# Kernel tuning notes

Measured on AMD Instinct MI355X. Metric: run time of the kernel, lower is better.

The kernel has to match this reference:

```python
import jax, jax.numpy as jnp
import numpy as np

D_MODEL = 96
D_STATE = 4
D_INNER = 192          # ssm_ratio * d_model
DT_RANK = 6            # ceil(d_model / 16)
K = 2                  # scan directions (fwd, reversed) over concatenated rgb||e sequence
D_CONV = 3
B, H, W = 2, 64, 64


def _layernorm(x, g, b, eps=1e-5):
    mu = jnp.mean(x, axis=-1, keepdims=True)
    var = jnp.mean((x - mu) ** 2, axis=-1, keepdims=True)
    return (x - mu) * jax.lax.rsqrt(var + eps) * g + b


def _dwconv(x, w, b):
    # x: [B, C, H, W], w: [C, 1, k, k] depthwise
    y = jax.lax.conv_general_dilated(
        x, w, window_strides=(1, 1), padding='SAME',
        feature_group_count=x.shape[1],
        dimension_numbers=('NCHW', 'OIHW', 'NCHW'))
    return y + b[None, :, None, None]


def setup_inputs() -> dict:
    key = jax.random.key(0)
    ks = jax.random.split(key, 16)
    f = lambda i, shape, s=0.02: jax.random.normal(ks[i], shape, dtype=jnp.float32) * s
    # dt_projs_bias mimics inverse-softplus of dt in [1e-3, 0.1]
    dt = jnp.exp(jax.random.uniform(ks[14], (K, D_INNER)) * (np.log(0.1) - np.log(0.001)) + np.log(0.001))
    inv_dt = dt + jnp.log(-jnp.expm1(-dt))
    return {
        'x_rgb': jax.random.normal(ks[0], (B, H, W, D_MODEL), jnp.float32),
        'x_e': jax.random.normal(ks[1], (B, H, W, D_MODEL), jnp.float32),
        'in_proj_w': f(2, (D_INNER, D_MODEL)),
        'in_proj_x_w': f(3, (D_INNER, D_MODEL)),
        'conv_w': f(4, (D_INNER, 1, D_CONV, D_CONV), 0.1),
        'conv_b': jnp.zeros((D_INNER,), jnp.float32),
        'conv_x_w': f(5, (D_INNER, 1, D_CONV, D_CONV), 0.1),
        'conv_x_b': jnp.zeros((D_INNER,), jnp.float32),
        'x_proj_weight': f(6, (K, DT_RANK + 2 * D_STATE, D_INNER)),
        'dt_projs_weight': f(7, (K, D_INNER, DT_RANK), DT_RANK ** -0.5),
        'dt_projs_bias': inv_dt.astype(jnp.float32),
        'A_logs': jnp.log(jnp.tile(jnp.arange(1, D_STATE + 1, dtype=jnp.float32)[None, :], (K * D_INNER, 1))),
        'Ds': jnp.ones((K * D_INNER,), jnp.float32),
        'ln1_g': jnp.ones((D_INNER,), jnp.float32), 'ln1_b': jnp.zeros((D_INNER,), jnp.float32),
        'ln2_g': jnp.ones((D_INNER,), jnp.float32), 'ln2_b': jnp.zeros((D_INNER,), jnp.float32),
        'out_proj_w': f(8, (D_MODEL, 2 * D_INNER)),
        'fc1_w1': f(9, (D_INNER // 16, D_INNER)), 'fc1_w2': f(10, (D_INNER, D_INNER // 16)),
        'fc2_w1': f(11, (D_INNER // 16, D_INNER)), 'fc2_w2': f(12, (D_INNER, D_INNER // 16)),
    }


def _mm_ss2d(x_rgb, x_e, in_proj_w, in_proj_x_w, conv_w, conv_b, conv_x_w, conv_x_b,
             x_proj_weight, dt_projs_weight, dt_projs_bias, A_logs, Ds,
             ln1_g, ln1_b, ln2_g, ln2_b, out_proj_w, fc1_w1, fc1_w2, fc2_w1, fc2_w2):
    # input projections (no bias)
    xr = x_rgb @ in_proj_w.T                       # [B,H,W,Di]
    xe = x_e @ in_proj_x_w.T
    xr_t = jnp.transpose(xr, (0, 3, 1, 2))         # [B,Di,H,W]
    xe_t = jnp.transpose(xe, (0, 3, 1, 2))
    xr_c = jax.nn.silu(_dwconv(xr_t, conv_w, conv_b))
    xe_c = jax.nn.silu(_dwconv(xe_t, conv_x_w, conv_x_b))

    Bb, Di, Hh, Ww = xr_c.shape
    HW = Hh * Ww
    # CrossScan_multimodal: concat rgb||e along sequence; K=2 = (forward, reversed)
    seq = jnp.concatenate([xr_c.reshape(Bb, Di, HW), xe_c.reshape(Bb, Di, HW)], axis=-1)  # [B,Di,2HW]
    xs = jnp.stack([seq, seq[..., ::-1]], axis=1)  # [B,K,Di,L]

    # projections for dt, B, C
    x_dbl = jnp.einsum('bkdl,kcd->bkcl', xs, x_proj_weight)
    dts, Bs, Cs = jnp.split(x_dbl, [DT_RANK, DT_RANK + D_STATE], axis=2)  # [B,K,R,L], [B,K,N,L] x2
    dts = jnp.einsum('bkrl,kdr->bkdl', dts, dt_projs_weight)
    delta = jax.nn.softplus(dts + dt_projs_bias.reshape(1, K, Di, 1))     # [B,K,Di,L]

    A = -jnp.exp(A_logs).reshape(K, Di, D_STATE)
    dA = jnp.exp(jnp.einsum('bkdl,kdn->bkdln', delta, A))                 # decay factors
    dBu = jnp.einsum('bkdl,bknl,bkdl->bkdln', delta, Bs, xs)              # driven input

    # S6 recurrence h_l = dA_l * h_{l-1} + dBu_l via parallel associative scan over L
    def combine(c1, c2):
        a1, b1 = c1
        a2, b2 = c2
        return a1 * a2, a2 * b1 + b2
    _, h = jax.lax.associative_scan(combine, (dA, dBu), axis=3)           # [B,K,Di,L,N]
    ys = jnp.einsum('bkdln,bknl->bkdl', h, Cs) + xs * Ds.reshape(1, K, Di, 1)

    # CrossMerge_multimodal: add reversed direction back, split modalities
    y = ys[:, 0] + ys[:, 1][..., ::-1]             # [B,Di,2HW]
    y_rgb = jnp.transpose(y[..., :HW], (0, 2, 1))  # [B,HW,Di]
    y_e = jnp.transpose(y[..., HW:], (0, 2, 1))
    y_rgb = _layernorm(y_rgb, ln1_g, ln1_b).reshape(Bb, Hh, Ww, Di)
    y_e = _layernorm(y_e, ln2_g, ln2_b).reshape(Bb, Hh, Ww, Di)

    # squeeze-excitation on pre-conv projected features
    sr = jnp.mean(xr_t, axis=(2, 3))               # [B,Di]
    se = jnp.mean(xe_t, axis=(2, 3))
    ex_r = jax.nn.sigmoid(jax.nn.silu(sr @ fc1_w1.T) @ fc1_w2.T)
    ex_e = jax.nn.sigmoid(jax.nn.silu(se @ fc2_w1.T) @ fc2_w2.T)
    y_rgb = y_rgb * ex_r[:, None, None, :]
    y_e = y_e * ex_e[:, None, None, :]

    yc = jnp.concatenate([y_rgb, y_e], axis=-1)    # [B,H,W,2Di]
    return yc @ out_proj_w.T                       # [B,H,W,d_model]


def reference(x_rgb, x_e, in_proj_w, in_proj_x_w, conv_w, conv_b, conv_x_w, conv_x_b,
              x_proj_weight, dt_projs_weight, dt_projs_bias, A_logs, Ds,
              ln1_g, ln1_b, ln2_g, ln2_b, out_proj_w, fc1_w1, fc1_w2, fc2_w1, fc2_w2):
    return _mm_ss2d(x_rgb, x_e, in_proj_w, in_proj_x_w, conv_w, conv_b, conv_x_w, conv_x_b,
                    x_proj_weight, dt_projs_weight, dt_projs_bias, A_logs, Ds,
                    ln1_g, ln1_b, ln2_g, ln2_b, out_proj_w, fc1_w1, fc1_w2, fc2_w1, fc2_w2)
```

## Files before the change

kernel.cpp:

```cpp
#include <hip/hip_runtime.h>
#include <math.h>

#define B_  2
#define H_  64
#define W_  64
#define HW  4096
#define DM  96
#define DI  192
#define NS  4
#define RK  6
#define KD  2
#define LL  8192

__device__ __forceinline__ float sigmoidf_(float x){ return 1.f/(1.f+__expf(-x)); }
__device__ __forceinline__ float4 rev4(float4 v){ return make_float4(v.w,v.z,v.y,v.x); }

__global__ void k_zero(float* __restrict__ p, int n){
  int i = blockIdx.x*256 + threadIdx.x;
  if (i < n) p[i] = 0.f;
}

__global__ __launch_bounds__(256) void k_inproj(
    const float* __restrict__ xrgb, const float* __restrict__ xe,
    const float* __restrict__ wr,   const float* __restrict__ we,
    float* __restrict__ xrt, float* __restrict__ xet, float* __restrict__ sr)
{
  __shared__ float lsW[DI*100];
  __shared__ float lsum[DI];
  const int mod = blockIdx.z, b = blockIdx.y;
  const int hw0 = blockIdx.x * 64;
  const float* x  = mod ? xe  : xrgb;
  const float* Wp = mod ? we  : wr;
  float* out      = mod ? xet : xrt;
  const int tid = threadIdx.x;
  for (int t = tid; t < DI*DM; t += 256){
    int di = t / DM, kk = t - di*DM;
    lsW[di*100 + kk] = Wp[t];
  }
  if (tid < DI) lsum[tid] = 0.f;
  const int cg = tid & 31, slot = tid >> 5;
  const int r0 = slot * 8;
  const float* xb = x + ((size_t)(b*HW) + hw0 + r0)*DM;
  float acc[8][6];
  #pragma unroll
  for (int i=0;i<8;i++)
    #pragma unroll
    for (int q=0;q<6;q++) acc[i][q]=0.f;
  __syncthreads();
  for (int kk4=0; kk4<DM/4; kk4++){
    float4 xv[8];
    #pragma unroll
    for (int i=0;i<8;i++) xv[i] = *(const float4*)(xb + (size_t)i*DM + kk4*4);
    #pragma unroll
    for (int q=0;q<6;q++){
      const float4 wv = *(const float4*)(&lsW[(cg+32*q)*100 + kk4*4]);
      #pragma unroll
      for (int i=0;i<8;i++){
        acc[i][q] = fmaf(xv[i].x, wv.x, acc[i][q]);
        acc[i][q] = fmaf(xv[i].y, wv.y, acc[i][q]);
        acc[i][q] = fmaf(xv[i].z, wv.z, acc[i][q]);
        acc[i][q] = fmaf(xv[i].w, wv.w, acc[i][q]);
      }
    }
  }
  #pragma unroll
  for (int q=0;q<6;q++){
    int di = cg + 32*q;
    float* ob = out + ((size_t)(b*DI + di))*HW + hw0 + r0;
    float ps = 0.f;
    #pragma unroll
    for (int i=0;i<8;i++){ ob[i] = acc[i][q]; ps += acc[i][q]; }
    atomicAdd(&lsum[di], ps);
  }
  __syncthreads();
  if (tid < DI) atomicAdd(&sr[((size_t)mod*B_ + b)*DI + tid], lsum[tid]);
}

__global__ __launch_bounds__(256) void k_conv(
    const float* __restrict__ xrt, const float* __restrict__ xet,
    const float* __restrict__ cwr, const float* __restrict__ cbr,
    const float* __restrict__ cwe, const float* __restrict__ cbe,
    float* __restrict__ seq)
{
  const int z = blockIdx.z; const int b = z >> 1, mod = z & 1;
  const int d = blockIdx.y;
  const float* in = (mod? xet:xrt) + ((size_t)b*DI + d)*HW;
  const float* wp = (mod? cwe:cwr) + d*9;
  const float  bias = (mod? cbe:cbr)[d];
  const int hw = blockIdx.x*256 + threadIdx.x;
  const int y = hw >> 6, x = hw & 63;
  float w[9];
  #pragma unroll
  for (int i=0;i<9;i++) w[i]=wp[i];
  float acc = bias;
  #pragma unroll
  for (int dy=-1;dy<=1;dy++){
    int yy = y+dy;
    if (yy<0||yy>=H_) continue;
    #pragma unroll
    for (int dx=-1;dx<=1;dx++){
      int xx = x+dx;
      if (xx<0||xx>=W_) continue;
      acc += in[yy*W_+xx]*w[(dy+1)*3 + dx+1];
    }
  }
  float v = acc * sigmoidf_(acc);
  seq[((size_t)b*DI + d)*LL + mod*HW + hw] = v;
}

__global__ void k_se(const float* __restrict__ sr,
                     const float* __restrict__ f11, const float* __restrict__ f12,
                     const float* __restrict__ f21, const float* __restrict__ f22,
                     float* __restrict__ ex)
{
  const int b = blockIdx.x, mod = blockIdx.y;
  const float* f1 = mod? f21:f11;
  const float* f2 = mod? f22:f12;
  __shared__ float s[DI];
  __shared__ float hid[12];
  const int t = threadIdx.x;
  s[t] = sr[((size_t)mod*B_ + b)*DI + t] * (1.f/HW);
  __syncthreads();
  if (t < 12){
    float a=0.f;
    for (int dd=0; dd<DI; dd++) a += f1[t*DI+dd]*s[dd];
    hid[t] = a * sigmoidf_(a);
  }
  __syncthreads();
  float a=0.f;
  #pragma unroll
  for (int h=0; h<12; h++) a += f2[t*12+h]*hid[h];
  ex[((size_t)mod*B_ + b)*DI + t] = sigmoidf_(a);
}

__global__ __launch_bounds__(256) void k_proj(
    const float* __restrict__ seq, const float* __restrict__ xpw,
    float* __restrict__ P)
{
  __shared__ float lw[14*DI];
  __shared__ float part[3][14][66];
  const int b = blockIdx.z, k = blockIdx.y;
  const int j0 = blockIdx.x*64;
  const int tid = threadIdx.x;
  const int jl = tid & 63, dq = tid >> 6;
  const int j = j0 + jl;
  for (int t = tid; t < 14*DI; t += 256) lw[t] = xpw[(size_t)k*14*DI + t];
  __syncthreads();
  float acc[14];
  #pragma unroll
  for (int c=0;c<14;c++) acc[c]=0.f;
  const float* sp = seq + (size_t)b*DI*LL + (size_t)(dq*48)*LL + j;
  const float* lwq = lw + dq*48;
  for (int dd=0; dd<48; dd++){
    float s = sp[(size_t)dd*LL];
    #pragma unroll
    for (int cc=0; cc<14; cc++) acc[cc] = fmaf(lwq[cc*DI+dd], s, acc[cc]);
  }
  if (dq){
    #pragma unroll
    for (int cc=0; cc<14; cc++) part[dq-1][cc][jl] = acc[cc];
  }
  __syncthreads();
  if (dq == 0){
    const int bk = b*KD + k;
    float* Pb = P + (size_t)bk*14*LL;
    #pragma unroll
    for (int cc=0; cc<14; cc++){
      float v = acc[cc] + part[0][cc][jl] + part[1][cc][jl] + part[2][cc][jl];
      Pb[(size_t)cc*LL + j] = v;
    }
  }
}

#define GETC(v_, s_) ((s_)==0?(v_).x:((s_)==1?(v_).y:((s_)==2?(v_).z:(v_).w)))
#define NT8 8

template<int KDIR>
__device__ __forceinline__ void scan_impl(
    const float* __restrict__ sq, const float* __restrict__ Pb,
    const float* A, const float* dwv, float bias, float Dv,
    float* __restrict__ yo, float (*wc)[4][8], int t)
{
  const int lane = t & 63, w = t >> 6;
  float cH[NS] = {0.f,0.f,0.f,0.f};

  for (int tt=0; tt<NT8; ++tt){
    const int j0 = KDIR ? (LL - 1024*tt - 4*t - 4) : (1024*tt + 4*t);
    float4 f0 = *(const float4*)(Pb + 0*(size_t)LL + j0);
    float4 f1 = *(const float4*)(Pb + 1*(size_t)LL + j0);
    float4 f2 = *(const float4*)(Pb + 2*(size_t)LL + j0);
    float4 f3 = *(const float4*)(Pb + 3*(size_t)LL + j0);
    float4 f4v= *(const float4*)(Pb + 4*(size_t)LL + j0);
    float4 f5 = *(const float4*)(Pb + 5*(size_t)LL + j0);
    float4 fx = *(const float4*)(sq + j0);
    float4 b0 = *(const float4*)(Pb + 6*(size_t)LL + j0);
    float4 b1 = *(const float4*)(Pb + 7*(size_t)LL + j0);
    float4 b2 = *(const float4*)(Pb + 8*(size_t)LL + j0);
    float4 b3 = *(const float4*)(Pb + 9*(size_t)LL + j0);
    float4 c0 = *(const float4*)(Pb + 10*(size_t)LL + j0);
    float4 c1 = *(const float4*)(Pb + 11*(size_t)LL + j0);
    float4 c2 = *(const float4*)(Pb + 12*(size_t)LL + j0);
    float4 c3 = *(const float4*)(Pb + 13*(size_t)LL + j0);
    if (KDIR){
      f0=rev4(f0); f1=rev4(f1); f2=rev4(f2); f3=rev4(f3); f4v=rev4(f4v); f5=rev4(f5);
      fx=rev4(fx);
      b0=rev4(b0); b1=rev4(b1); b2=rev4(b2); b3=rev4(b3);
      c0=rev4(c0); c1=rev4(c1); c2=rev4(c2); c3=rev4(c3);
    }

    float del[4], du[4];
    #pragma unroll
    for (int i=0;i<4;i++){
      float acc = bias;
      acc = fmaf(dwv[0],GETC(f0,i),acc); acc = fmaf(dwv[1],GETC(f1,i),acc);
      acc = fmaf(dwv[2],GETC(f2,i),acc); acc = fmaf(dwv[3],GETC(f3,i),acc);
      acc = fmaf(dwv[4],GETC(f4v,i),acc); acc = fmaf(dwv[5],GETC(f5,i),acc);
      del[i] = (acc > 20.f) ? acc : __logf(1.f + __expf(acc));
      du[i]  = del[i]*GETC(fx,i);
    }

    float lA[NS][4], lH[NS][4];
    #pragma unroll
    for (int n=0;n<NS;n++){
      float rA=1.f, rH=0.f;
      #pragma unroll
      for (int i=0;i<4;i++){
        float Bi = GETC((n==0?b0:n==1?b1:n==2?b2:b3), i);
        float ai = __expf(del[i]*A[n]);
        rH = fmaf(ai, rH, du[i]*Bi);
        rA *= ai;
        lA[n][i]=rA; lH[n][i]=rH;
      }
    }

    float sA[NS], sH[NS];
    #pragma unroll
    for (int n=0;n<NS;n++){ sA[n]=lA[n][3]; sH[n]=lH[n][3]; }
    #pragma unroll
    for (int s=1; s<64; s<<=1){
      float pa[NS], ph[NS];
      #pragma unroll
      for (int n=0;n<NS;n++){ pa[n]=__shfl_up(sA[n],(unsigned)s,64); ph[n]=__shfl_up(sH[n],(unsigned)s,64); }
      if (lane >= s){
        #pragma unroll
        for (int n=0;n<NS;n++){ sH[n]=fmaf(sA[n],ph[n],sH[n]); sA[n]*=pa[n]; }
      }
    }
    float eA[NS], eH[NS];
    #pragma unroll
    for (int n=0;n<NS;n++){
      float xa = __shfl_up(sA[n],1u,64), xh = __shfl_up(sH[n],1u,64);
      eA[n] = lane ? xa : 1.f;
      eH[n] = lane ? xh : 0.f;
    }

    const int buf = tt & 1;
    if (lane == 63){
      #pragma unroll
      for (int n=0;n<NS;n++){ wc[buf][w][n]=sA[n]; wc[buf][w][4+n]=sH[n]; }
    }
    __syncthreads();

    float WA[NS]={1.f,1.f,1.f,1.f}, WH[NS]={0.f,0.f,0.f,0.f};
    float TA[NS]={1.f,1.f,1.f,1.f}, TH[NS]={0.f,0.f,0.f,0.f};
    #pragma unroll
    for (int ww=0; ww<4; ww++){
      #pragma unroll
      for (int n=0;n<NS;n++){
        float qa = wc[buf][ww][n], qh = wc[buf][ww][4+n];
        if (ww < w){ WH[n]=fmaf(qa,WH[n],qh); WA[n]*=qa; }
        TH[n]=fmaf(qa,TH[n],qh); TA[n]*=qa;
      }
    }

    float PH[NS];
    #pragma unroll
    for (int n=0;n<NS;n++){
      float GH = fmaf(WA[n], cH[n], WH[n]);
      PH[n] = fmaf(eA[n], GH, eH[n]);
    }

    float yv[4];
    #pragma unroll
    for (int i=0;i<4;i++){
      float y = Dv*GETC(fx,i);
      #pragma unroll
      for (int n=0;n<NS;n++){
        float h = fmaf(lA[n][i], PH[n], lH[n][i]);
        float Ci = GETC((n==0?c0:n==1?c1:n==2?c2:c3), i);
        y = fmaf(Ci, h, y);
      }
      yv[i] = y;
    }
    float4 o = make_float4(yv[0],yv[1],yv[2],yv[3]);
    if (KDIR) o = rev4(o);
    *(float4*)(yo + j0) = o;

    #pragma unroll
    for (int n=0;n<NS;n++) cH[n] = fmaf(TA[n], cH[n], TH[n]);
  }
}

__global__ __launch_bounds__(256, 3) void k_scan(
    const float* __restrict__ seq,  const float* __restrict__ P,
    const float* __restrict__ dtw,  const float* __restrict__ dtb,
    const float* __restrict__ Alogs,const float* __restrict__ Dsp,
    float* __restrict__ y0, float* __restrict__ y1)
{
  const int gid = blockIdx.x;
  const int d = gid % DI;
  const int k = (gid / DI) % KD;
  const int b = gid / (DI*KD);
  const int t = threadIdx.x;
  const int kd = k*DI + d;
  float A[NS];
  #pragma unroll
  for (int n=0;n<NS;n++) A[n] = -__expf(Alogs[kd*NS+n]);
  float dwv[RK];
  #pragma unroll
  for (int r=0;r<RK;r++) dwv[r] = dtw[kd*RK+r];
  const float bias = dtb[kd];
  const float Dv   = Dsp[kd];
  const float* sq = seq + ((size_t)b*DI + d)*LL;
  const int bk = b*KD + k;
  const float* Pb = P + (size_t)bk*14*LL;
  float* yo = (k ? y1 : y0) + ((size_t)b*DI + d)*LL;

  __shared__ float wc[2][4][8];

  if (k == 0) scan_impl<0>(sq, Pb, A, dwv, bias, Dv, yo, wc, t);
  else        scan_impl<1>(sq, Pb, A, dwv, bias, Dv, yo, wc, t);
}

__global__ __launch_bounds__(256) void k_ln(
    const float* __restrict__ y0, const float* __restrict__ y1,
    const float* __restrict__ ln1g, const float* __restrict__ ln1b,
    const float* __restrict__ ln2g, const float* __restrict__ ln2b,
    const float* __restrict__ ex, float* __restrict__ yln)
{
  const int b  = blockIdx.y;
  const int j0 = blockIdx.x*64;
  __shared__ float v[DI][65];
  __shared__ float ps1[4][64], ps2[4][64];
  __shared__ float mu[64], rs[64];
  const int tid = threadIdx.x;
  const int jl = tid & 63, ds = tid >> 6;
  const float* p0 = y0 + (size_t)b*DI*LL + j0;
  const float* p1 = y1 + (size_t)b*DI*LL + j0;
  for (int it=0; it<48; it++){
    int d = ds*48 + it;
    v[d][jl] = p0[(size_t)d*LL + jl] + p1[(size_t)d*LL + jl];
  }
  __syncthreads();
  float s1=0.f, s2=0.f;
  for (int it=0; it<48; it++){
    float x = v[ds*48+it][jl];
    s1 += x; s2 += x*x;
  }
  ps1[ds][jl]=s1; ps2[ds][jl]=s2;
  __syncthreads();
  if (tid < 64){
    float t1 = ps1[0][tid]+ps1[1][tid]+ps1[2][tid]+ps1[3][tid];
    float t2 = ps2[0][tid]+ps2[1][tid]+ps2[2][tid]+ps2[3][tid];
    float m  = t1*(1.f/DI);
    float var= t2*(1.f/DI) - m*m;
    mu[tid]=m; rs[tid]=rsqrtf(var + 1e-5f);
  }
  __syncthreads();
  const int mod = (j0 >= HW) ? 1 : 0;
  const float* g  = mod? ln2g:ln1g;
  const float* bb = mod? ln2b:ln1b;
  const float* exm = ex + ((size_t)mod*B_ + b)*DI;
  for (int it=0; it<48; it++){
    int idx = it*256 + tid;
    int j = idx / DI;
    int d = idx - j*DI;
    float x = v[d][j];
    float o = (x - mu[j])*rs[j]*g[d] + bb[d];
    o *= exm[d];
    yln[((size_t)b*LL + j0 + j)*DI + d] = o;
  }
}

__global__ __launch_bounds__(128) void k_out(
    const float* __restrict__ yln, const float* __restrict__ Wo, float* __restrict__ out)
{
  __shared__ float lsW[DM*68];
  const int bid  = blockIdx.x;
  const int ks   = bid & 1;
  const int rg   = bid >> 1;
  const int row0 = rg * 32;
  const int b    = row0 >> 12;
  const int hw0  = row0 & (HW-1);
  const int tid  = threadIdx.x;
  const int cg = tid & 31, slot = tid >> 5;
  const int r0 = slot * 8;
  float acc[8][3];
  #pragma unroll
  for (int i=0;i<8;i++)
    #pragma unroll
    for (int q=0;q<3;q++) acc[i][q]=0.f;

  const float* xrow = yln + ((size_t)b*LL + (ks ? HW+hw0 : hw0) + r0)*DI;
  for (int c=0;c<3;c++){
    const int colbase = ks*192 + c*64;
    for (int t=tid; t<DM*64; t+=128){
      int dm = t>>6, kkl = t&63;
      lsW[dm*68 + kkl] = Wo[(size_t)dm*384 + colbase + kkl];
    }
    __syncthreads();
    const float* xb = xrow + c*64;
    for (int kk4=0; kk4<16; kk4++){
      float4 xv[8];
      #pragma unroll
      for (int i=0;i<8;i++) xv[i] = *(const float4*)(xb + (size_t)i*DI + kk4*4);
      #pragma unroll
      for (int q=0;q<3;q++){
        const float4 wv = *(const float4*)(&lsW[(cg+32*q)*68 + kk4*4]);
        #pragma unroll
        for (int i=0;i<8;i++){
          acc[i][q] = fmaf(xv[i].x, wv.x, acc[i][q]);
          acc[i][q] = fmaf(xv[i].y, wv.y, acc[i][q]);
          acc[i][q] = fmaf(xv[i].z, wv.z, acc[i][q]);
          acc[i][q] = fmaf(xv[i].w, wv.w, acc[i][q]);
        }
      }
    }
    __syncthreads();
  }
  #pragma unroll
  for (int i=0;i<8;i++){
    float* ob = out + (size_t)(row0 + r0 + i)*DM;
    #pragma unroll
    for (int q=0;q<3;q++) atomicAdd(&ob[cg + 32*q], acc[i][q]);
  }
}

extern "C" void kernel_launch(void* const* d_in, const int* in_sizes, int n_in,
                              void* d_out, int out_size, void* d_ws, size_t ws_size,
                              hipStream_t stream) {
  const float* x_rgb      = (const float*)d_in[0];
  const float* x_e        = (const float*)d_in[1];
  const float* in_proj_w  = (const float*)d_in[2];
  const float* in_proj_xw = (const float*)d_in[3];
  const float* conv_w     = (const float*)d_in[4];
  const float* conv_b     = (const float*)d_in[5];
  const float* conv_xw    = (const float*)d_in[6];
  const float* conv_xb    = (const float*)d_in[7];
  const float* xpw        = (const float*)d_in[8];
  const float* dtw        = (const float*)d_in[9];
  const float* dtb        = (const float*)d_in[10];
  const float* A_logs     = (const float*)d_in[11];
  const float* Ds         = (const float*)d_in[12];
  const float* ln1_g      = (const float*)d_in[13];
  const float* ln1_b      = (const float*)d_in[14];
  const float* ln2_g      = (const float*)d_in[15];
  const float* ln2_b      = (const float*)d_in[16];
  const float* out_proj_w = (const float*)d_in[17];
  const float* fc1_w1     = (const float*)d_in[18];
  const float* fc1_w2     = (const float*)d_in[19];
  const float* fc2_w1     = (const float*)d_in[20];
  const float* fc2_w2     = (const float*)d_in[21];

  float* ws = (float*)d_ws;
  float* xr_t = ws;
  float* xe_t = ws + 1572864;
  float* y0   = ws;
  float* seq  = ws + 3145728;
  float* yln  = seq;
  float* y1   = ws + 6291456;
  float* P    = ws + 9437184;
  float* sr   = ws + 9895936;
  float* ex   = ws + 9896704;
  float* outp = (float*)d_out;

  k_zero  <<<dim3(3), 256, 0, stream>>>(sr, 768);
  k_inproj<<<dim3(HW/64, B_, 2), 256, 0, stream>>>(x_rgb, x_e, in_proj_w, in_proj_xw, xr_t, xe_t, sr);
  k_conv  <<<dim3(HW/256, DI, B_*2), 256, 0, stream>>>(xr_t, xe_t, conv_w, conv_b, conv_xw, conv_xb, seq);
  k_se    <<<dim3(B_, 2), DI, 0, stream>>>(sr, fc1_w1, fc1_w2, fc2_w1, fc2_w2, ex);
  k_proj  <<<dim3(LL/64, KD, B_), 256, 0, stream>>>(seq, xpw, P);
  k_scan  <<<dim3(B_*KD*DI), 256, 0, stream>>>(seq, P, dtw, dtb, A_logs, Ds, y0, y1);
  k_ln    <<<dim3(LL/64, B_), 256, 0, stream>>>(y0, y1, ln1_g, ln1_b, ln2_g, ln2_b, ex, yln);
  k_zero  <<<dim3((B_*HW*DM + 255)/256), 256, 0, stream>>>(outp, B_*HW*DM);
  k_out   <<<dim3(512), 128, 0, stream>>>(yln, out_proj_w, outp);
}
```

Measured before the change: 139.5 us.

## Fuse layernorm into out-projection and use integer-power decay in scan

Merges the LayerNorm+SE-scale kernel into the output projection kernel, so each block sums y0+y1, normalizes its 32 rows in shared memory and multiplies them by Wo directly. This removes the yln round-trip to global memory and one launch. The scan also checks at runtime whether A equals -[1,2,3,4]. If so, it computes exp(delta*A_n) as powers of 1/(1+e^acc), which replaces four exps per element with one reciprocal and a few multiplies. The fast path is taken only when A_logs matches log(1..4), and the fused kernel uses more shared memory per block.

```diff
diff --git a/kernel.cpp b/kernel.cpp
--- a/kernel.cpp
+++ b/kernel.cpp
@@ -175,7 +175,7 @@
 #define GETC(v_, s_) ((s_)==0?(v_).x:((s_)==1?(v_).y:((s_)==2?(v_).z:(v_).w)))
 #define NT8 8
 
-template<int KDIR>
+template<int KDIR, bool IPOW>
 __device__ __forceinline__ void scan_impl(
     const float* __restrict__ sq, const float* __restrict__ Pb,
     const float* A, const float* dwv, float bias, float Dv,
@@ -208,14 +208,26 @@
       c0=rev4(c0); c1=rev4(c1); c2=rev4(c2); c3=rev4(c3);
     }
 
-    float del[4], du[4];
+    float del[4], du[4], aP0[4], aP1[4], aP2[4], aP3[4];
     #pragma unroll
     for (int i=0;i<4;i++){
       float acc = bias;
       acc = fmaf(dwv[0],GETC(f0,i),acc); acc = fmaf(dwv[1],GETC(f1,i),acc);
       acc = fmaf(dwv[2],GETC(f2,i),acc); acc = fmaf(dwv[3],GETC(f3,i),acc);
       acc = fmaf(dwv[4],GETC(f4v,i),acc); acc = fmaf(dwv[5],GETC(f5,i),acc);
-      del[i] = (acc > 20.f) ? acc : __logf(1.f + __expf(acc));
+      if (IPOW){
+        float ex_ = __expf(acc);
+        float dl  = (acc > 20.f) ? acc : __logf(1.f + ex_);
+        del[i] = dl;
+        float a0 = 1.f/(1.f + ex_);
+        float a1 = a0*a0;
+        aP0[i]=a0; aP1[i]=a1; aP2[i]=a1*a0; aP3[i]=a1*a1;
+      } else {
+        float dl = (acc > 20.f) ? acc : __logf(1.f + __expf(acc));
+        del[i] = dl;
+        aP0[i]=__expf(dl*A[0]); aP1[i]=__expf(dl*A[1]);
+        aP2[i]=__expf(dl*A[2]); aP3[i]=__expf(dl*A[3]);
+      }
       du[i]  = del[i]*GETC(fx,i);
     }
 
@@ -226,7 +238,7 @@
       #pragma unroll
       for (int i=0;i<4;i++){
         float Bi = GETC((n==0?b0:n==1?b1:n==2?b2:b3), i);
-        float ai = __expf(del[i]*A[n]);
+        float ai = (n==0? aP0[i] : n==1? aP1[i] : n==2? aP2[i] : aP3[i]);
         rH = fmaf(ai, rH, du[i]*Bi);
         rA *= ai;
         lA[n][i]=rA; lH[n][i]=rH;
@@ -328,97 +340,102 @@
 
   __shared__ float wc[2][4][8];
 
-  if (k == 0) scan_impl<0>(sq, Pb, A, dwv, bias, Dv, yo, wc, t);
-  else        scan_impl<1>(sq, Pb, A, dwv, bias, Dv, yo, wc, t);
-}
-
-__global__ __launch_bounds__(256) void k_ln(
+  const float tol = 1e-5f * fabsf(A[0]);
+  const bool ipow = (fabsf(A[1]-2.f*A[0])<tol) && (fabsf(A[2]-3.f*A[0])<tol)
+                 && (fabsf(A[3]-4.f*A[0])<tol) && (fabsf(A[0]+1.f) < 1e-5f);
+
+  if (ipow){
+    if (k == 0) scan_impl<0,true>(sq, Pb, A, dwv, bias, Dv, yo, wc, t);
+    else        scan_impl<1,true>(sq, Pb, A, dwv, bias, Dv, yo, wc, t);
+  } else {
+    if (k == 0) scan_impl<0,false>(sq, Pb, A, dwv, bias, Dv, yo, wc, t);
+    else        scan_impl<1,false>(sq, Pb, A, dwv, bias, Dv, yo, wc, t);
+  }
+}
+
+#define LNP 200
+__global__ __launch_bounds__(256) void k_outln(
     const float* __restrict__ y0, const float* __restrict__ y1,
     const float* __restrict__ ln1g, const float* __restrict__ ln1b,
     const float* __restrict__ ln2g, const float* __restrict__ ln2b,
-    const float* __restrict__ ex, float* __restrict__ yln)
-{
-  const int b  = blockIdx.y;
-  const int j0 = blockIdx.x*64;
-  __shared__ float v[DI][65];
-  __shared__ float ps1[4][64], ps2[4][64];
-  __shared__ float mu[64], rs[64];
-  const int tid = threadIdx.x;
-  const int jl = tid & 63, ds = tid >> 6;
-  const float* p0 = y0 + (size_t)b*DI*LL + j0;
-  const float* p1 = y1 + (size_t)b*DI*LL + j0;
-  for (int it=0; it<48; it++){
-    int d = ds*48 + it;
-    v[d][jl] = p0[(size_t)d*LL + jl] + p1[(size_t)d*LL + jl];
-  }
-  __syncthreads();
-  float s1=0.f, s2=0.f;
-  for (int it=0; it<48; it++){
-    float x = v[ds*48+it][jl];
-    s1 += x; s2 += x*x;
-  }
-  ps1[ds][jl]=s1; ps2[ds][jl]=s2;
-  __syncthreads();
-  if (tid < 64){
-    float t1 = ps1[0][tid]+ps1[1][tid]+ps1[2][tid]+ps1[3][tid];
-    float t2 = ps2[0][tid]+ps2[1][tid]+ps2[2][tid]+ps2[3][tid];
-    float m  = t1*(1.f/DI);
-    float var= t2*(1.f/DI) - m*m;
-    mu[tid]=m; rs[tid]=rsqrtf(var + 1e-5f);
-  }
-  __syncthreads();
-  const int mod = (j0 >= HW) ? 1 : 0;
-  const float* g  = mod? ln2g:ln1g;
-  const float* bb = mod? ln2b:ln1b;
-  const float* exm = ex + ((size_t)mod*B_ + b)*DI;
-  for (int it=0; it<48; it++){
-    int idx = it*256 + tid;
-    int j = idx / DI;
-    int d = idx - j*DI;
-    float x = v[d][j];
-    float o = (x - mu[j])*rs[j]*g[d] + bb[d];
-    o *= exm[d];
-    yln[((size_t)b*LL + j0 + j)*DI + d] = o;
-  }
-}
-
-__global__ __launch_bounds__(128) void k_out(
-    const float* __restrict__ yln, const float* __restrict__ Wo, float* __restrict__ out)
-{
+    const float* __restrict__ ex,  const float* __restrict__ Wo,
+    float* __restrict__ out)
+{
+  __shared__ float vx[32][LNP];
   __shared__ float lsW[DM*68];
-  const int bid  = blockIdx.x;
-  const int ks   = bid & 1;
-  const int rg   = bid >> 1;
+  __shared__ float ps1[8][33], ps2[8][33];
+  __shared__ float lmu[32], lrs[32];
+  __shared__ float lgx[DI], lbx[DI];
+
+  const int bid = blockIdx.x;
+  const int ks  = bid & 1;
+  const int rg  = bid >> 1;
   const int row0 = rg * 32;
   const int b    = row0 >> 12;
   const int hw0  = row0 & (HW-1);
+  const int seq0 = ks*HW + hw0;
   const int tid  = threadIdx.x;
+  const int jl = tid & 31, dg = tid >> 5;
+
+  {
+    const float* g  = ks? ln2g : ln1g;
+    const float* bb = ks? ln2b : ln1b;
+    const float* exm = ex + ((size_t)ks*B_ + b)*DI;
+    if (tid < DI){ float e = exm[tid]; lgx[tid] = g[tid]*e; lbx[tid] = bb[tid]*e; }
+  }
+
+  const float* p0 = y0 + (size_t)b*DI*LL + seq0;
+  const float* p1 = y1 + (size_t)b*DI*LL + seq0;
+  float s1=0.f, s2=0.f;
+  for (int i=0;i<24;i++){
+    int di = dg*24 + i;
+    float v = p0[(size_t)di*LL + jl] + p1[(size_t)di*LL + jl];
+    vx[jl][di] = v;
+    s1 += v; s2 += v*v;
+  }
+  ps1[dg][jl]=s1; ps2[dg][jl]=s2;
+  __syncthreads();
+  if (tid < 32){
+    float t1=0.f, t2=0.f;
+    #pragma unroll
+    for (int q=0;q<8;q++){ t1+=ps1[q][tid]; t2+=ps2[q][tid]; }
+    float m  = t1*(1.f/DI);
+    float var= t2*(1.f/DI) - m*m;
+    lmu[tid]=m; lrs[tid]=rsqrtf(var + 1e-5f);
+  }
+  __syncthreads();
+  {
+    float m = lmu[jl], r = lrs[jl];
+    for (int i=0;i<24;i++){
+      int di = dg*24 + i;
+      vx[jl][di] = fmaf((vx[jl][di]-m)*r, lgx[di], lbx[di]);
+    }
+  }
+  __syncthreads();
+
   const int cg = tid & 31, slot = tid >> 5;
-  const int r0 = slot * 8;
-  float acc[8][3];
-  #pragma unroll
-  for (int i=0;i<8;i++)
+  const int r0 = slot * 4;
+  float acc[4][3];
+  #pragma unroll
+  for (int i=0;i<4;i++)
     #pragma unroll
     for (int q=0;q<3;q++) acc[i][q]=0.f;
 
-  const float* xrow = yln + ((size_t)b*LL + (ks ? HW+hw0 : hw0) + r0)*DI;
   for (int c=0;c<3;c++){
-    const int colbase = ks*192 + c*64;
-    for (int t=tid; t<DM*64; t+=128){
+    for (int t=tid; t<DM*64; t+=256){
       int dm = t>>6, kkl = t&63;
-      lsW[dm*68 + kkl] = Wo[(size_t)dm*384 + colbase + kkl];
+      lsW[dm*68 + kkl] = Wo[(size_t)dm*384 + ks*192 + c*64 + kkl];
     }
     __syncthreads();
-    const float* xb = xrow + c*64;
     for (int kk4=0; kk4<16; kk4++){
-      float4 xv[8];
-      #pragma unroll
-      for (int i=0;i<8;i++) xv[i] = *(const float4*)(xb + (size_t)i*DI + kk4*4);
+      float4 xv[4];
+      #pragma unroll
+      for (int i=0;i<4;i++) xv[i] = *(const float4*)(&vx[r0+i][c*64 + kk4*4]);
       #pragma unroll
       for (int q=0;q<3;q++){
         const float4 wv = *(const float4*)(&lsW[(cg+32*q)*68 + kk4*4]);
         #pragma unroll
-        for (int i=0;i<8;i++){
+        for (int i=0;i<4;i++){
           acc[i][q] = fmaf(xv[i].x, wv.x, acc[i][q]);
           acc[i][q] = fmaf(xv[i].y, wv.y, acc[i][q]);
           acc[i][q] = fmaf(xv[i].z, wv.z, acc[i][q]);
@@ -429,7 +446,7 @@
     __syncthreads();
   }
   #pragma unroll
-  for (int i=0;i<8;i++){
+  for (int i=0;i<4;i++){
     float* ob = out + (size_t)(row0 + r0 + i)*DM;
     #pragma unroll
     for (int q=0;q<3;q++) atomicAdd(&ob[cg + 32*q], acc[i][q]);
@@ -467,7 +484,6 @@
   float* xe_t = ws + 1572864;
   float* y0   = ws;
   float* seq  = ws + 3145728;
-  float* yln  = seq;
   float* y1   = ws + 6291456;
   float* P    = ws + 9437184;
   float* sr   = ws + 9895936;
@@ -480,7 +496,6 @@
   k_se    <<<dim3(B_, 2), DI, 0, stream>>>(sr, fc1_w1, fc1_w2, fc2_w1, fc2_w2, ex);
   k_proj  <<<dim3(LL/64, KD, B_), 256, 0, stream>>>(seq, xpw, P);
   k_scan  <<<dim3(B_*KD*DI), 256, 0, stream>>>(seq, P, dtw, dtb, A_logs, Ds, y0, y1);
-  k_ln    <<<dim3(LL/64, B_), 256, 0, stream>>>(y0, y1, ln1_g, ln1_b, ln2_g, ln2_b, ex, yln);
   k_zero  <<<dim3((B_*HW*DM + 255)/256), 256, 0, stream>>>(outp, B_*HW*DM);
-  k_out   <<<dim3(512), 128, 0, stream>>>(yln, out_proj_w, outp);
-}
+  k_outln <<<dim3(512), 256, 0, stream>>>(y0, y1, ln1_g, ln1_b, ln2_g, ln2_b, ex, out_proj_w, outp);
+}
```

After: 425.3 us. 3.05x slower.
